# Optimization experiments

Hardware: AMD Instinct MI355X
Metric: run time of the kernel (lower is better)

The kernel has to match this reference:

```python
import jax, jax.numpy as jnp
import numpy as np

B, L, P = 16, 128, 8192
ALPHA = 2.0            # current_alpha (softness_start)
STEP_PROGRESS = 0.5    # > 0.15 so e_ghost == 0; t_gate = sigmoid(3.0)
PROT_RADII = np.array([1.7, 1.55, 1.52, 1.8], dtype=np.float32)
PROT_EPS = np.array([0.1, 0.1, 0.15, 0.2], dtype=np.float32)
VDW_RADII = np.array([1.7, 1.55, 1.52, 1.8, 1.1, 1.47, 1.75, 1.85, 1.98], dtype=np.float32)
EPSILON = np.array([0.086, 0.17, 0.21, 0.25, 0.015, 0.061, 0.265, 0.32, 0.4], dtype=np.float32)


def setup_inputs() -> dict:
    key = jax.random.key(0)
    ks = jax.random.split(key, 6)
    # positions spread over ~ a binding-pocket-sized box so distances are realistic
    pos_L = jax.random.normal(ks[0], (B, L, 3), jnp.float32) * 8.0
    pos_P = jax.random.normal(ks[1], (B, P, 3), jnp.float32) * 8.0
    q_L = jax.random.normal(ks[2], (B, L), jnp.float32) * 0.3
    q_P = jax.random.normal(ks[3], (B, P), jnp.float32) * 0.3
    x_L = jax.random.uniform(ks[4], (B, L, 9), jnp.float32)
    x_L = x_L / jnp.sum(x_L, axis=-1, keepdims=True)  # type probabilities
    x_P = jax.random.uniform(ks[5], (B, P, 4), jnp.float32)
    x_P = x_P / jnp.sum(x_P, axis=-1, keepdims=True)
    return {
        'pos_L': pos_L, 'pos_P': pos_P, 'q_L': q_L, 'q_P': q_P,
        'x_L': x_L, 'x_P': x_P,
        'vdw_radii': jnp.asarray(VDW_RADII), 'epsilon_tbl': jnp.asarray(EPSILON),
    }


def reference(pos_L, pos_P, q_L, q_P, x_L, x_P, vdw_radii, epsilon_tbl):
    sg = jax.lax.stop_gradient
    # pairwise geometry: diff [B,L,P,3]
    diff = pos_L[:, :, None, :] - pos_P[:, None, :, :]
    dist_sq = jnp.sum(diff * diff, axis=-1)              # [B,L,P]
    dist = jnp.sqrt(dist_sq + 1e-8)
    # mixed vdw radii
    type_probs_L = x_L[..., :9]
    radii_L = type_probs_L @ vdw_radii                    # [B,L]
    radii_P = x_P[..., :4] @ jnp.asarray(PROT_RADII)      # [B,P]
    sigma_ij = radii_L[:, :, None] + radii_P[:, None, :]  # [B,L,P]
    # soft-core distance
    soft_dist = jnp.sqrt(dist_sq + ALPHA * sigma_ij * sigma_ij + 1e-8)
    # electrostatics (dielectric = 4.0), tanh-clamped
    e_elec_raw = 332.06 * q_L[:, :, None] * q_P[:, None, :] / (4.0 * soft_dist)
    e_elec = 200.0 * jnp.tanh(e_elec_raw / 200.0)
    # LJ 12-6 with geometric-mean epsilon
    eps_L = jax.nn.relu(type_probs_L @ epsilon_tbl)       # [B,L]
    eps_P = x_P[..., :4] @ jnp.asarray(PROT_EPS)          # [B,P]
    eps_ij = jnp.sqrt(eps_L[:, :, None] * eps_P[:, None, :] + 1e-8)
    ratio = jnp.minimum(sigma_ij / (soft_dist + 1e-8), 5.0)
    ratio6 = ratio ** 6
    ratio12 = ratio6 * ratio6
    e_vdw_raw = 4.0 * eps_ij * (ratio12 - ratio6)
    e_pos = 500.0 * jnp.tanh(jax.nn.relu(e_vdw_raw) / 500.0)
    e_neg = -10.0 * jnp.tanh(jax.nn.relu(-e_vdw_raw) / 10.0)
    e_vdw_grad = e_pos + e_neg
    # smooth 12 A cutoff
    dist_mask = jax.nn.sigmoid((12.0 - dist) * 2.0)
    e_soft = jnp.sum((e_elec + e_vdw_grad) * dist_mask, axis=(1, 2))  # [B]
    # hydrophobic surface attraction (carbon-carbon)
    mask_cc = type_probs_L[..., 0][:, :, None] * x_P[..., 0][:, None, :]
    hsa_term = 1.0 / (1.0 + (dist / 4.0) ** 4)
    e_hsa = jnp.sum(-0.5 * mask_cc * hsa_term * dist_mask, axis=(1, 2))
    # Pauli repulsion, gated by step progress
    t_gate = jax.nn.sigmoid(jnp.float32((STEP_PROGRESS - 0.2) * 10.0))
    overlap = jax.nn.relu(sigma_ij * 0.6 - dist)
    e_pauli = t_gate * 100.0 * jnp.sum(overlap * overlap, axis=(1, 2))
    # e_ghost = 0 since STEP_PROGRESS >= 0.15
    e_ghost = jnp.zeros_like(e_pauli)
    e_raw = e_soft + 5.0 * e_hsa + e_pauli + e_ghost
    e_raw = jnp.nan_to_num(e_raw, nan=0.0)
    # logging quantities (detached in the original)
    log_vdw = jnp.clip(sg(e_vdw_raw), -10.0, 500.0)
    log_soft_core = jnp.sum((sg(e_elec) + log_vdw) * sg(dist_mask), axis=(1, 2))
    e_soft_log = jnp.clip(log_soft_core + 5.0 * sg(e_hsa), -500.0, 5000.0)
    e_hard_log = jnp.minimum(sg(e_pauli + e_ghost), 10000.0)
    log_energy_val = jnp.minimum(e_soft_log + e_hard_log, 1000000.0)
    return e_raw, e_hard_log, jnp.float32(ALPHA), log_energy_val
```

## Files before the change

kernel.cpp:

```cpp
#include <hip/hip_runtime.h>
#include <math.h>
#include <stdint.h>

#define NB 16
#define NL 128
#define NP 8192
#define CHUNKS 32
#define THREADS 256
#define LSPLIT 4
#define LPB 16
#define NPAIR 64

typedef float v2 __attribute__((ext_vector_type(2)));
typedef float v4 __attribute__((ext_vector_type(4)));
typedef const __attribute__((address_space(4))) v4* cv4p;

__device__ __forceinline__ float fexp2(float x) { return __builtin_amdgcn_exp2f(x); }
__device__ __forceinline__ float frcp(float x)  { return __builtin_amdgcn_rcpf(x); }
__device__ __forceinline__ float frsq(float x)  { return __builtin_amdgcn_rsqf(x); }
__device__ __forceinline__ float fsqrt_(float x){ return __builtin_amdgcn_sqrtf(x); }
__device__ __forceinline__ v2 vfma(v2 a, v2 b, v2 c) { return __builtin_elementwise_fma(a, b, c); }

__global__ __launch_bounds__(256) void lig_prep(
    const float* __restrict__ pos_L, const float* __restrict__ q_L,
    const float* __restrict__ x_L,
    const float* __restrict__ vdw_radii, const float* __restrict__ eps_tbl,
    float* __restrict__ ligbuf)
{
    const int id = blockIdx.x * 256 + threadIdx.x;
    if (id >= NB * NL) return;
    const int b = id >> 7, l = id & 127;
    const int base = b * NL + l;
    float px = pos_L[base * 3 + 0];
    float py = pos_L[base * 3 + 1];
    float pz = pos_L[base * 3 + 2];
    float aq = 83.015f * q_L[base];
    float rad = 0.0f, ep = 0.0f;
    #pragma unroll
    for (int j = 0; j < 9; ++j) {
        float v = x_L[base * 9 + j];
        rad = fmaf(v, vdw_radii[j], rad);
        ep  = fmaf(v, eps_tbl[j],  ep);
    }
    float se4 = 4.0f * fsqrt_(fmaxf(ep, 0.0f));
    float x0  = x_L[base * 9 + 0];
    const int pair = l >> 1, s = l & 1;
    float* dst = ligbuf + ((size_t)(b * NPAIR + pair)) * 16;
    dst[ 0 + s] = px;
    dst[ 2 + s] = py;
    dst[ 4 + s] = pz;
    dst[ 6 + s] = aq;
    dst[ 8 + s] = rad;
    dst[10 + s] = se4;
    dst[12 + s] = x0;
    dst[14 + s] = 0.0f;
}

__global__ __launch_bounds__(THREADS) void physics_main(
    const float* __restrict__ pos_P, const float* __restrict__ q_P,
    const float* __restrict__ x_P,   const float* __restrict__ ligbuf,
    float* __restrict__ partial)
{
    const int b     = blockIdx.y;
    const int chunk = blockIdx.x;
    const int z     = blockIdx.z;
    const int tid   = threadIdx.x;

    __shared__ float red[4][3];

    const int pb = b * NP + chunk * THREADS + tid;
    const float ppx = pos_P[pb * 3 + 0];
    const float ppy = pos_P[pb * 3 + 1];
    const float ppz = pos_P[pb * 3 + 2];
    const float qP  = q_P[pb];
    const float4 xp = ((const float4*)x_P)[pb];
    const float rP  = 1.7f * xp.x + 1.55f * xp.y + 1.52f * xp.z + 1.8f * xp.w;
    const float epP = 0.1f * xp.x + 0.10f * xp.y + 0.15f * xp.z + 0.2f * xp.w;
    const float seP = fsqrt_(epP);
    const float xP0 = xp.x;

    v2 ppx2; ppx2.x = ppx; ppx2.y = ppx;
    v2 ppy2; ppy2.x = ppy; ppy2.y = ppy;
    v2 ppz2; ppz2.x = ppz; ppz2.y = ppz;
    v2 qP2;  qP2.x  = qP;  qP2.y  = qP;
    v2 rP2;  rP2.x  = rP;  rP2.y  = rP;
    v2 seP2; seP2.x = seP; seP2.y = seP;
    const v2 onev = (v2)1.0f;
    const v2 C1 = (v2)(-8.3333333e-6f);
    const v2 K1 = (v2)(2.8853901f);
    const v2 K2 = (v2)(-34.624681f);
    const v2 KQ = (v2)(0.0625f);
    const v2 KO = (v2)(0.6f);

    v2 s1v = (v2)0.0f, s2v = (v2)0.0f, s3v = (v2)0.0f;

    const float* lp = ligbuf + ((size_t)(b * NPAIR + z * LPB)) * 16;
    cv4p Lc = (cv4p)(uintptr_t)lp;

    #pragma unroll
    for (int i = 0; i < LPB; ++i) {
        const v4 A0 = Lc[i * 4 + 0];
        const v4 A1 = Lc[i * 4 + 1];
        const v4 A2 = Lc[i * 4 + 2];
        const v4 A3 = Lc[i * 4 + 3];

        v2 lx;   lx.x = A0.x;   lx.y = A0.y;
        v2 ly;   ly.x = A0.z;   ly.y = A0.w;
        v2 lz;   lz.x = A1.x;   lz.y = A1.y;
        v2 laq;  laq.x = A1.z;  laq.y = A1.w;
        v2 lrad; lrad.x = A2.x; lrad.y = A2.y;
        v2 lse;  lse.x = A2.z;  lse.y = A2.w;
        v2 lx0;  lx0.x = A3.x;  lx0.y = A3.y;

        v2 dx = lx - ppx2, dy = ly - ppy2, dz = lz - ppz2;
        v2 ds = vfma(dx, dx, vfma(dy, dy, vfma(dz, dz, (v2)1e-8f)));
        v2 dist; dist.x = fsqrt_(ds.x); dist.y = fsqrt_(ds.y);

        v2 sigma = lrad + rP2;
        v2 sigsq = sigma * sigma;
        v2 sd2 = vfma(sigsq, (v2)2.0f, ds);
        v2 inv; inv.x = frsq(sd2.x); inv.y = frsq(sd2.y);

        v2 v = (laq * qP2) * inv;
        v2 w = v * v;
        v2 e_elec = v * vfma(w, C1, onev);

        v2 inv2 = inv * inv;
        v2 r2 = sigsq * inv2;
        v2 r6 = r2 * r2 * r2;
        v2 t126 = vfma(r6, r6, -r6);
        v2 ev = (lse * seP2) * t126;
        v2 addend = e_elec + ev;

        v2 m = vfma(dist, K1, K2);
        v2 A; A.x = fexp2(m.x); A.y = fexp2(m.y);
        A = A + onev;
        v2 tq = ds * KQ;
        v2 Bh = vfma(tq, tq, onev);
        v2 AB = A * Bh;
        v2 r; r.x = frcp(AB.x); r.y = frcp(AB.y);
        v2 dm = Bh * r;

        s1v = vfma(addend, dm, s1v);
        s2v = vfma(lx0, r, s2v);
        v2 ov = __builtin_elementwise_max(vfma(sigma, KO, -dist), (v2)0.0f);
        s3v = vfma(ov, ov, s3v);
    }

    float s1 = s1v.x + s1v.y;
    float s2 = (s2v.x + s2v.y) * xP0;
    float s3 = s3v.x + s3v.y;

    #pragma unroll
    for (int off = 32; off > 0; off >>= 1) {
        s1 += __shfl_down(s1, off);
        s2 += __shfl_down(s2, off);
        s3 += __shfl_down(s3, off);
    }
    const int lane = tid & 63;
    const int wid  = tid >> 6;
    if (lane == 0) { red[wid][0] = s1; red[wid][1] = s2; red[wid][2] = s3; }
    __syncthreads();
    if (tid == 0) {
        float r0 = red[0][0] + red[1][0] + red[2][0] + red[3][0];
        float r1 = red[0][1] + red[1][1] + red[2][1] + red[3][1];
        float r2_ = red[0][2] + red[1][2] + red[2][2] + red[3][2];
        float* dst = partial + ((size_t)((b * CHUNKS + chunk) * LSPLIT + z)) * 4;
        dst[0] = r0; dst[1] = r1; dst[2] = r2_;
    }
}

__global__ __launch_bounds__(256) void physics_final(
    const float* __restrict__ partial, float* __restrict__ out)
{
    const int tid = threadIdx.x;
    if (tid == 0) out[2 * NB] = 2.0f;
    const int b = tid >> 4;
    const int j = tid & 15;
    float s1 = 0.0f, s2 = 0.0f, s3 = 0.0f;
    const int NPART = CHUNKS * LSPLIT;
    #pragma unroll
    for (int k = 0; k < NPART / 16; ++k) {
        const float* src = partial + ((size_t)(b * NPART + j * (NPART / 16) + k)) * 4;
        s1 += src[0]; s2 += src[1]; s3 += src[2];
    }
    #pragma unroll
    for (int off = 8; off > 0; off >>= 1) {
        s1 += __shfl_down(s1, off, 16);
        s2 += __shfl_down(s2, off, 16);
        s3 += __shfl_down(s3, off, 16);
    }
    if (j == 0) {
        const float TG100 = 95.25741268224334f;
        float e_pauli = TG100 * s3;
        float e_hsa5  = -2.5f * s2;
        float e_raw = s1 + e_hsa5 + e_pauli;
        if (e_raw != e_raw) e_raw = 0.0f;
        float e_hard_log = fminf(e_pauli, 10000.0f);
        float e_soft_log = fminf(fmaxf(s1 + e_hsa5, -500.0f), 5000.0f);
        float log_energy = fminf(e_soft_log + e_hard_log, 1000000.0f);
        out[b]              = e_raw;
        out[NB + b]         = e_hard_log;
        out[2 * NB + 1 + b] = log_energy;
    }
}

extern "C" void kernel_launch(void* const* d_in, const int* in_sizes, int n_in,
                              void* d_out, int out_size, void* d_ws, size_t ws_size,
                              hipStream_t stream)
{
    const float* pos_L = (const float*)d_in[0];
    const float* pos_P = (const float*)d_in[1];
    const float* q_L   = (const float*)d_in[2];
    const float* q_P   = (const float*)d_in[3];
    const float* x_L   = (const float*)d_in[4];
    const float* x_P   = (const float*)d_in[5];
    const float* vdw   = (const float*)d_in[6];
    const float* epst  = (const float*)d_in[7];
    float* out = (float*)d_out;

    float* ligbuf  = (float*)d_ws;
    float* partial = ligbuf + (size_t)NB * NPAIR * 16;

    lig_prep<<<8, 256, 0, stream>>>(pos_L, q_L, x_L, vdw, epst, ligbuf);
    dim3 grid(CHUNKS, NB, LSPLIT);
    physics_main<<<grid, THREADS, 0, stream>>>(pos_P, q_P, x_P, ligbuf, partial);
    physics_final<<<1, 256, 0, stream>>>(partial, out);
}
```

Baseline: 91.29 us.

## Vectorize over two protein atoms per thread with broadcast ligand scalars

```diff
diff --git a/kernel.cpp b/kernel.cpp
--- a/kernel.cpp
+++ b/kernel.cpp
@@ -5,11 +5,11 @@
 #define NB 16
 #define NL 128
 #define NP 8192
-#define CHUNKS 32
+#define CHUNKS 16
 #define THREADS 256
-#define LSPLIT 4
+#define PPT 2
+#define LSPLIT 8
 #define LPB 16
-#define NPAIR 64
 
 typedef float v2 __attribute__((ext_vector_type(2)));
 typedef float v4 __attribute__((ext_vector_type(4)));
@@ -29,8 +29,7 @@
 {
     const int id = blockIdx.x * 256 + threadIdx.x;
     if (id >= NB * NL) return;
-    const int b = id >> 7, l = id & 127;
-    const int base = b * NL + l;
+    const int base = id;
     float px = pos_L[base * 3 + 0];
     float py = pos_L[base * 3 + 1];
     float pz = pos_L[base * 3 + 2];
@@ -44,16 +43,9 @@
     }
     float se4 = 4.0f * fsqrt_(fmaxf(ep, 0.0f));
     float x0  = x_L[base * 9 + 0];
-    const int pair = l >> 1, s = l & 1;
-    float* dst = ligbuf + ((size_t)(b * NPAIR + pair)) * 16;
-    dst[ 0 + s] = px;
-    dst[ 2 + s] = py;
-    dst[ 4 + s] = pz;
-    dst[ 6 + s] = aq;
-    dst[ 8 + s] = rad;
-    dst[10 + s] = se4;
-    dst[12 + s] = x0;
-    dst[14 + s] = 0.0f;
+    float4* dst = (float4*)(ligbuf + (size_t)base * 8);
+    dst[0] = make_float4(px, py, pz, aq);
+    dst[1] = make_float4(rad, se4, x0, 0.0f);
 }
 
 __global__ __launch_bounds__(THREADS) void physics_main(
@@ -68,60 +60,50 @@
 
     __shared__ float red[4][3];
 
-    const int pb = b * NP + chunk * THREADS + tid;
-    const float ppx = pos_P[pb * 3 + 0];
-    const float ppy = pos_P[pb * 3 + 1];
-    const float ppz = pos_P[pb * 3 + 2];
-    const float qP  = q_P[pb];
-    const float4 xp = ((const float4*)x_P)[pb];
-    const float rP  = 1.7f * xp.x + 1.55f * xp.y + 1.52f * xp.z + 1.8f * xp.w;
-    const float epP = 0.1f * xp.x + 0.10f * xp.y + 0.15f * xp.z + 0.2f * xp.w;
-    const float seP = fsqrt_(epP);
-    const float xP0 = xp.x;
-
-    v2 ppx2; ppx2.x = ppx; ppx2.y = ppx;
-    v2 ppy2; ppy2.x = ppy; ppy2.y = ppy;
-    v2 ppz2; ppz2.x = ppz; ppz2.y = ppz;
-    v2 qP2;  qP2.x  = qP;  qP2.y  = qP;
-    v2 rP2;  rP2.x  = rP;  rP2.y  = rP;
-    v2 seP2; seP2.x = seP; seP2.y = seP;
+    const int p0  = chunk * (THREADS * PPT) + tid;
+    const int pb0 = b * NP + p0;
+    const int pb1 = pb0 + THREADS;
+
+    v2 ppx2; ppx2.x = pos_P[pb0 * 3 + 0]; ppx2.y = pos_P[pb1 * 3 + 0];
+    v2 ppy2; ppy2.x = pos_P[pb0 * 3 + 1]; ppy2.y = pos_P[pb1 * 3 + 1];
+    v2 ppz2; ppz2.x = pos_P[pb0 * 3 + 2]; ppz2.y = pos_P[pb1 * 3 + 2];
+    v2 qP2;  qP2.x  = q_P[pb0];           qP2.y  = q_P[pb1];
+    const float4 xp0 = ((const float4*)x_P)[pb0];
+    const float4 xp1 = ((const float4*)x_P)[pb1];
+    v2 rP2, seP2, xP02;
+    rP2.x  = 1.7f * xp0.x + 1.55f * xp0.y + 1.52f * xp0.z + 1.8f * xp0.w;
+    rP2.y  = 1.7f * xp1.x + 1.55f * xp1.y + 1.52f * xp1.z + 1.8f * xp1.w;
+    seP2.x = fsqrt_(0.1f * xp0.x + 0.10f * xp0.y + 0.15f * xp0.z + 0.2f * xp0.w);
+    seP2.y = fsqrt_(0.1f * xp1.x + 0.10f * xp1.y + 0.15f * xp1.z + 0.2f * xp1.w);
+    xP02.x = xp0.x; xP02.y = xp1.x;
+
     const v2 onev = (v2)1.0f;
     const v2 C1 = (v2)(-8.3333333e-6f);
     const v2 K1 = (v2)(2.8853901f);
     const v2 K2 = (v2)(-34.624681f);
-    const v2 KQ = (v2)(0.0625f);
-    const v2 KO = (v2)(0.6f);
 
     v2 s1v = (v2)0.0f, s2v = (v2)0.0f, s3v = (v2)0.0f;
 
-    const float* lp = ligbuf + ((size_t)(b * NPAIR + z * LPB)) * 16;
+    const float* lp = ligbuf + ((size_t)(b * NL + z * LPB)) * 8;
     cv4p Lc = (cv4p)(uintptr_t)lp;
 
     #pragma unroll
     for (int i = 0; i < LPB; ++i) {
-        const v4 A0 = Lc[i * 4 + 0];
-        const v4 A1 = Lc[i * 4 + 1];
-        const v4 A2 = Lc[i * 4 + 2];
-        const v4 A3 = Lc[i * 4 + 3];
-
-        v2 lx;   lx.x = A0.x;   lx.y = A0.y;
-        v2 ly;   ly.x = A0.z;   ly.y = A0.w;
-        v2 lz;   lz.x = A1.x;   lz.y = A1.y;
-        v2 laq;  laq.x = A1.z;  laq.y = A1.w;
-        v2 lrad; lrad.x = A2.x; lrad.y = A2.y;
-        v2 lse;  lse.x = A2.z;  lse.y = A2.w;
-        v2 lx0;  lx0.x = A3.x;  lx0.y = A3.y;
-
-        v2 dx = lx - ppx2, dy = ly - ppy2, dz = lz - ppz2;
+        const v4 A0 = Lc[i * 2 + 0];
+        const v4 A1 = Lc[i * 2 + 1];
+
+        v2 dx = (v2)A0.x - ppx2;
+        v2 dy = (v2)A0.y - ppy2;
+        v2 dz = (v2)A0.z - ppz2;
         v2 ds = vfma(dx, dx, vfma(dy, dy, vfma(dz, dz, (v2)1e-8f)));
         v2 dist; dist.x = fsqrt_(ds.x); dist.y = fsqrt_(ds.y);
 
-        v2 sigma = lrad + rP2;
+        v2 sigma = (v2)A1.x + rP2;
         v2 sigsq = sigma * sigma;
         v2 sd2 = vfma(sigsq, (v2)2.0f, ds);
         v2 inv; inv.x = frsq(sd2.x); inv.y = frsq(sd2.y);
 
-        v2 v = (laq * qP2) * inv;
+        v2 v = ((v2)A0.w * qP2) * inv;
         v2 w = v * v;
         v2 e_elec = v * vfma(w, C1, onev);
 
@@ -129,26 +111,27 @@
         v2 r2 = sigsq * inv2;
         v2 r6 = r2 * r2 * r2;
         v2 t126 = vfma(r6, r6, -r6);
-        v2 ev = (lse * seP2) * t126;
+        v2 ev = ((v2)A1.y * seP2) * t126;
         v2 addend = e_elec + ev;
 
         v2 m = vfma(dist, K1, K2);
         v2 A; A.x = fexp2(m.x); A.y = fexp2(m.y);
         A = A + onev;
-        v2 tq = ds * KQ;
+        v2 tq = ds * 0.0625f;
         v2 Bh = vfma(tq, tq, onev);
         v2 AB = A * Bh;
-        v2 r; r.x = frcp(AB.x); r.y = frcp(AB.y);
-        v2 dm = Bh * r;
+        v2 rr; rr.x = frcp(AB.x); rr.y = frcp(AB.y);
+        v2 dm = Bh * rr;
 
         s1v = vfma(addend, dm, s1v);
-        s2v = vfma(lx0, r, s2v);
-        v2 ov = __builtin_elementwise_max(vfma(sigma, KO, -dist), (v2)0.0f);
+        s2v = vfma((v2)A1.z, rr, s2v);
+        v2 ov = __builtin_elementwise_max(vfma(sigma, (v2)0.6f, -dist), (v2)0.0f);
         s3v = vfma(ov, ov, s3v);
     }
 
+    v2 s2p = s2v * xP02;
     float s1 = s1v.x + s1v.y;
-    float s2 = (s2v.x + s2v.y) * xP0;
+    float s2 = s2p.x + s2p.y;
     float s3 = s3v.x + s3v.y;
 
     #pragma unroll
@@ -220,7 +203,7 @@
     float* out = (float*)d_out;
 
     float* ligbuf  = (float*)d_ws;
-    float* partial = ligbuf + (size_t)NB * NPAIR * 16;
+    float* partial = ligbuf + (size_t)NB * NL * 8;
 
     lig_prep<<<8, 256, 0, stream>>>(pos_L, q_L, x_L, vdw, epst, ligbuf);
     dim3 grid(CHUNKS, NB, LSPLIT);
```

Result: faster. 88.27 us (-3.3%).
